# Optimization experiments

Measured on AMD Instinct MI355X. Metric: run time of the kernel, lower is better.

## Reference

```python
import jax, jax.numpy as jnp
import numpy as np

N_USERS = 4096
N_ITEMS = 4096
D = 64  # embedding_dim / out_features
N = N_USERS + N_ITEMS
ALPHA = 0.2  # LeakyReLU slope
NEG_INF = jnp.float32(-9e15)


def setup_inputs() -> dict:
    key = jax.random.key(0)
    ks = jax.random.split(key, 11)
    s = 0.05  # xavier-ish scale
    rn = lambda k, shape: jax.random.normal(k, shape, jnp.float32) * s
    adj = jax.random.randint(ks[0], (N, N), 0, 2, jnp.int32)
    return {
        "adj": adj,
        "user_emb": rn(ks[1], (N_USERS, D)),
        "item_emb": rn(ks[2], (N_ITEMS, D)),
        "W0_w": rn(ks[3], (D, D)), "W0_b": rn(ks[4], (D,)), "a0": rn(ks[5], (2 * D, 1)),
        "W1_w": rn(ks[6], (D, D)), "W1_b": rn(ks[7], (D,)), "a1": rn(ks[8], (2 * D, 1)),
        "out_w": rn(ks[9], (D, D)), "out_b": rn(ks[10], (D,)),
    }


def gat_layer(x, adj, W_w, W_b, a):
    # Wh: [N, D]
    Wh = x @ W_w.T + W_b
    # Original materializes [N,N,2D] concat then matmul with a.
    # Algebraically identical: e_ij = leakyrelu(a1 . Wh_i + a2 . Wh_j)
    src = Wh @ a[:D]          # [N, 1] -> row contribution
    dst = (Wh @ a[D:]).T      # [1, N] -> column contribution
    e = jax.nn.leaky_relu(src + dst, ALPHA)        # [N, N]
    e = jnp.where(adj > 0, e, NEG_INF)
    att = jax.nn.softmax(e, axis=1)                # dropout=0.0 (eval)
    return att @ Wh                                 # [N, D]


def reference(adj, user_emb, item_emb, W0_w, W0_b, a0, W1_w, W1_b, a1, out_w, out_b):
    x = jnp.concatenate([user_emb, item_emb], axis=0)  # [N, D]
    x = jax.nn.relu(gat_layer(x, adj, W0_w, W0_b, a0))
    x = jax.nn.relu(gat_layer(x, adj, W1_w, W1_b, a1))
    u, it = x[:N_USERS], x[N_USERS:]
    return (u @ out_w.T + out_b, it @ out_w.T + out_b)
```

## Files before the change

### kernel.cpp

```cpp
#include <hip/hip_runtime.h>


typedef __attribute__((ext_vector_type(8))) __bf16 bf16x8;
typedef __attribute__((ext_vector_type(4))) float  f32x4;

union Frag {
    bf16x8         v;
    unsigned int   w[4];
    unsigned short h[8];
};

__device__ __forceinline__ unsigned short f2bf(float f) {
    unsigned int u = __float_as_uint(f);
    u += 0x7FFFu + ((u >> 16) & 1u);
    return (unsigned short)(u >> 16);
}

__device__ __forceinline__ void prep_tail(
    float (*xs)[65], float (*Wt)[65], float (*sred)[64], float (*dred)[64],
    const float* __restrict__ W, const float* __restrict__ bias,
    const float* __restrict__ avec,
    unsigned short* __restrict__ WhT, float* __restrict__ sraw,
    float* __restrict__ draw, int tid, int r0)
{
    for (int e = tid; e < 4096; e += 256) {
        int o = e >> 6, c = e & 63;
        Wt[c][o] = W[e];
    }
    __syncthreads();

    int r = tid & 63, chunk = tid >> 6, c0 = chunk * 16;
    float acc[16];
#pragma unroll
    for (int o = 0; o < 16; o++) acc[o] = bias[c0 + o];
    for (int c = 0; c < 64; c++) {
        float xv = xs[r][c];
#pragma unroll
        for (int o = 0; o < 16; o++) acc[o] += xv * Wt[c][c0 + o];
    }

    float sp = 0.f, dp = 0.f;
#pragma unroll
    for (int o = 0; o < 16; o++) {
        sp += acc[o] * avec[c0 + o];
        dp += acc[o] * avec[64 + c0 + o];
    }
    sred[chunk][r] = sp;
    dred[chunk][r] = dp;

#pragma unroll
    for (int o = 0; o < 16; o++)
        WhT[(c0 + o) * 8192 + r0 + r] = f2bf(acc[o]);

    __syncthreads();
    if (tid < 64) {
        int g = r0 + tid;
        sraw[g] = sred[0][tid] + sred[1][tid] + sred[2][tid] + sred[3][tid];
        draw[g] = dred[0][tid] + dred[1][tid] + dred[2][tid] + dred[3][tid];
    }
}

__global__ __launch_bounds__(256) void k_prep0(
    const float* __restrict__ ue, const float* __restrict__ ie,
    const float* __restrict__ W, const float* __restrict__ bias,
    const float* __restrict__ avec,
    unsigned short* __restrict__ WhT,
    float* __restrict__ sraw, float* __restrict__ draw)
{
    __shared__ float xs[64][65];
    __shared__ float Wt[64][65];
    __shared__ float sred[4][64];
    __shared__ float dred[4][64];
    int tid = threadIdx.x, r0 = blockIdx.x * 64;

    for (int e = tid; e < 4096; e += 256) {
        int r = e >> 6, c = e & 63;
        int row = r0 + r;
        xs[r][c] = (row < 4096) ? ue[row * 64 + c] : ie[(row - 4096) * 64 + c];
    }
    prep_tail(xs, Wt, sred, dred, W, bias, avec, WhT, sraw, draw, tid, r0);
}

template <int NS>
__global__ __launch_bounds__(256) void k_prep1(
    const float* __restrict__ numP, const float* __restrict__ denP,
    const float* __restrict__ W, const float* __restrict__ bias,
    const float* __restrict__ avec,
    unsigned short* __restrict__ WhT,
    float* __restrict__ sraw, float* __restrict__ draw)
{
    __shared__ float xs[64][65];
    __shared__ float Wt[64][65];
    __shared__ float sred[4][64];
    __shared__ float dred[4][64];
    __shared__ float dtot[64];
    int tid = threadIdx.x, r0 = blockIdx.x * 64;

    if (tid < 64) {
        float s = 0.f;
#pragma unroll
        for (int p = 0; p < NS; p++) s += denP[p * 8192 + r0 + tid];
        dtot[tid] = fmaxf(s, 1e-20f);
    }
    __syncthreads();
    for (int e = tid; e < 4096; e += 256) {
        int r = e >> 6, c = e & 63;
        float s = 0.f;
#pragma unroll
        for (int p = 0; p < NS; p++)
            s += numP[(size_t)p * 524288 + (r0 + r) * 64 + c];
        float v = s / dtot[r];
        xs[r][c] = v > 0.f ? v : 0.f;
    }
    prep_tail(xs, Wt, sred, dred, W, bias, avec, WhT, sraw, draw, tid, r0);
}

template <int RAW, int NSPLIT>
__global__ __launch_bounds__(256, 8) void k_agg(
    const int* __restrict__ adj, unsigned int* __restrict__ adjbits,
    const unsigned short* __restrict__ WhT,
    const float* __restrict__ sraw, const float* __restrict__ draw,
    float* __restrict__ numP, float* __restrict__ denP)
{
    const int KR = 8192 / NSPLIT;
    int tid  = threadIdx.x;
    int wave = tid >> 6, lane = tid & 63;
    int quad = lane >> 4, l16 = lane & 15;
    int rowblk = blockIdx.x, ks = blockIdx.y;
    int row = rowblk * 64 + wave * 16 + l16;
    int k0  = ks * KR;

    float sv = sraw[row];

    f32x4 accs[4];
    f32x4 accd = {0.f, 0.f, 0.f, 0.f};
#pragma unroll
    for (int nt = 0; nt < 4; nt++) accs[nt] = accd;

    Frag ones;
    ones.w[0] = ones.w[1] = ones.w[2] = ones.w[3] = 0x3F803F80u;

    for (int kb = k0; kb < k0 + KR; kb += 32) {
        int kq = kb + quad * 8;

        unsigned int mask8;
        if constexpr (RAW) {
            const int4* ap = reinterpret_cast<const int4*>(adj + (size_t)row * 8192 + kq);
            int4 a0 = ap[0], a1 = ap[1];
            int ai[8] = {a0.x, a0.y, a0.z, a0.w, a1.x, a1.y, a1.z, a1.w};
            mask8 = 0;
#pragma unroll
            for (int j = 0; j < 8; j++)
                if (ai[j] != 0) mask8 |= (1u << j);
            reinterpret_cast<unsigned char*>(adjbits)[(size_t)row * 1024 + (kb >> 3) + quad] =
                (unsigned char)mask8;
        } else {
            unsigned int word = adjbits[row * 256 + (kb >> 5)];
            mask8 = (word >> (quad * 8)) & 0xFFu;
        }

        float4 dd0 = *reinterpret_cast<const float4*>(draw + kq);
        float4 dd1 = *reinterpret_cast<const float4*>(draw + kq + 4);
        float dv[8] = {dd0.x, dd0.y, dd0.z, dd0.w, dd1.x, dd1.y, dd1.z, dd1.w};

        Frag A;
#pragma unroll
        for (int j = 0; j < 8; j++) {
            float t  = sv + dv[j];
            float lr = t > 0.f ? t : 0.2f * t;
            float w  = ((mask8 >> j) & 1u) ? __expf(lr) : 0.f;
            A.h[j] = f2bf(w);
        }

#pragma unroll
        for (int nt = 0; nt < 4; nt++) {
            Frag B;
            B.v = *reinterpret_cast<const bf16x8*>(WhT + (size_t)(nt * 16 + l16) * 8192 + kq);
            accs[nt] = __builtin_amdgcn_mfma_f32_16x16x32_bf16(A.v, B.v, accs[nt], 0, 0, 0);
        }
        accd = __builtin_amdgcn_mfma_f32_16x16x32_bf16(A.v, ones.v, accd, 0, 0, 0);
    }

    int rbase = rowblk * 64 + wave * 16 + quad * 4;
    size_t nb = (size_t)ks * 524288;
#pragma unroll
    for (int rr = 0; rr < 4; rr++) {
        if (l16 == 0) denP[ks * 8192 + rbase + rr] = accd[rr];
#pragma unroll
        for (int nt = 0; nt < 4; nt++)
            numP[nb + (size_t)(rbase + rr) * 64 + nt * 16 + l16] = accs[nt][rr];
    }
}

template <int NS>
__global__ __launch_bounds__(256) void k_out(
    const float* __restrict__ numP, const float* __restrict__ denP,
    const float* __restrict__ W, const float* __restrict__ bias,
    float* __restrict__ out)
{
    __shared__ float xs[64][65];
    __shared__ float Wt[64][65];
    __shared__ float dtot[64];
    int tid = threadIdx.x, r0 = blockIdx.x * 64;

    if (tid < 64) {
        float s = 0.f;
#pragma unroll
        for (int p = 0; p < NS; p++) s += denP[p * 8192 + r0 + tid];
        dtot[tid] = fmaxf(s, 1e-20f);
    }
    __syncthreads();
    for (int e = tid; e < 4096; e += 256) {
        int r = e >> 6, c = e & 63;
        float s = 0.f;
#pragma unroll
        for (int p = 0; p < NS; p++)
            s += numP[(size_t)p * 524288 + (r0 + r) * 64 + c];
        float v = s / dtot[r];
        xs[r][c] = v > 0.f ? v : 0.f;
    }
    for (int e = tid; e < 4096; e += 256) {
        int o = e >> 6, c = e & 63;
        Wt[c][o] = W[e];
    }
    __syncthreads();

    int r = tid & 63, chunk = tid >> 6, c0 = chunk * 16;
    float acc[16];
#pragma unroll
    for (int o = 0; o < 16; o++) acc[o] = bias[c0 + o];
    for (int c = 0; c < 64; c++) {
        float xv = xs[r][c];
#pragma unroll
        for (int o = 0; o < 16; o++) acc[o] += xv * Wt[c][c0 + o];
    }
#pragma unroll
    for (int o = 0; o < 16; o++)
        out[(r0 + r) * 64 + c0 + o] = acc[o];
}

extern "C" void kernel_launch(void* const* d_in, const int* in_sizes, int n_in,
                              void* d_out, int out_size, void* d_ws, size_t ws_size,
                              hipStream_t stream)
{
    const int*   adj = (const int*)d_in[0];
    const float* ue  = (const float*)d_in[1];
    const float* ie  = (const float*)d_in[2];
    const float* W0w = (const float*)d_in[3];
    const float* W0b = (const float*)d_in[4];
    const float* a0  = (const float*)d_in[5];
    const float* W1w = (const float*)d_in[6];
    const float* W1b = (const float*)d_in[7];
    const float* a1  = (const float*)d_in[8];
    const float* Ow  = (const float*)d_in[9];
    const float* Ob  = (const float*)d_in[10];

    constexpr int NS0 = 16, NS1 = 8;

    char* ws = (char*)d_ws;
    size_t off = 0;
    auto alloc = [&](size_t bytes) -> char* {
        char* p = ws + off;
        off += (bytes + 255) & ~(size_t)255;
        return p;
    };
    float*          numP    = (float*)alloc((size_t)NS0 * 524288 * 4);
    float*          denP    = (float*)alloc((size_t)NS0 * 8192 * 4);
    unsigned int*   adjbits = (unsigned int*)alloc(8192 * 1024);
    unsigned short* WhT0    = (unsigned short*)alloc(64 * 8192 * 2);
    unsigned short* WhT1    = (unsigned short*)alloc(64 * 8192 * 2);
    float* sr0 = (float*)alloc(8192 * 4);
    float* dr0 = (float*)alloc(8192 * 4);
    float* sr1 = (float*)alloc(8192 * 4);
    float* dr1 = (float*)alloc(8192 * 4);

    k_prep0<<<128, 256, 0, stream>>>(ue, ie, W0w, W0b, a0, WhT0, sr0, dr0);
    k_agg<1, NS0><<<dim3(128, NS0), 256, 0, stream>>>(adj, adjbits, WhT0,
                                                      sr0, dr0, numP, denP);
    k_prep1<NS0><<<128, 256, 0, stream>>>(numP, denP, W1w, W1b, a1, WhT1, sr1, dr1);
    k_agg<0, NS1><<<dim3(128, NS1), 256, 0, stream>>>((const int*)nullptr, adjbits, WhT1,
                                                      sr1, dr1, numP, denP);
    k_out<NS1><<<128, 256, 0, stream>>>(numP, denP, Ow, Ob, (float*)d_out);
}
```

Baseline: 573.1 us.

## Factor attention exp into per-node terms, stage Wh in LDS with fp16 MFMA

Rewrites the attention weight as max(exp(s_i)exp(d_j), exp(0.2 s_i)exp(0.2 d_j)), precomputed per node in prep, so the inner loop needs only packed fp16 multiplies and a max instead of a per-element exp. The aggregation kernel now packs the adjacency mask with wave ballots into shared memory, double-buffers Wh tiles in LDS, and uses fp16 MFMA instead of bf16. Layer 0 now uses 8 K-splits instead of 16, and partial outputs are written in a block-contiguous layout through an LDS transpose. The risk is fp16 overflow or underflow of the exponent products when scores are large, and reduced parallelism in layer 0.

```diff
diff --git a/kernel.cpp b/kernel.cpp
--- a/kernel.cpp
+++ b/kernel.cpp
@@ -1,27 +1,28 @@
 #include <hip/hip_runtime.h>
 
 
-typedef __attribute__((ext_vector_type(8))) __bf16 bf16x8;
-typedef __attribute__((ext_vector_type(4))) float  f32x4;
-
-union Frag {
-    bf16x8         v;
-    unsigned int   w[4];
-    unsigned short h[8];
+typedef _Float16 f16x8 __attribute__((ext_vector_type(8)));
+typedef _Float16 f16x2 __attribute__((ext_vector_type(2)));
+typedef __attribute__((ext_vector_type(4))) float f32x4;
+
+union Frag16 {
+    f16x8        v;
+    unsigned int u[4];
 };
-
-__device__ __forceinline__ unsigned short f2bf(float f) {
-    unsigned int u = __float_as_uint(f);
-    u += 0x7FFFu + ((u >> 16) & 1u);
-    return (unsigned short)(u >> 16);
-}
+union HV2 {
+    f16x2        v;
+    _Float16     h[2];
+    unsigned int u;
+};
 
 __device__ __forceinline__ void prep_tail(
     float (*xs)[65], float (*Wt)[65], float (*sred)[64], float (*dred)[64],
     const float* __restrict__ W, const float* __restrict__ bias,
     const float* __restrict__ avec,
-    unsigned short* __restrict__ WhT, float* __restrict__ sraw,
-    float* __restrict__ draw, int tid, int r0)
+    _Float16* __restrict__ WhT,
+    unsigned int* __restrict__ E12,
+    _Float16* __restrict__ F1h, _Float16* __restrict__ F2h,
+    int tid, int r0)
 {
     for (int e = tid; e < 4096; e += 256) {
         int o = e >> 6, c = e & 63;
@@ -50,13 +51,19 @@
 
 #pragma unroll
     for (int o = 0; o < 16; o++)
-        WhT[(c0 + o) * 8192 + r0 + r] = f2bf(acc[o]);
+        WhT[(size_t)(c0 + o) * 8192 + r0 + r] = (_Float16)acc[o];
 
     __syncthreads();
     if (tid < 64) {
         int g = r0 + tid;
-        sraw[g] = sred[0][tid] + sred[1][tid] + sred[2][tid] + sred[3][tid];
-        draw[g] = dred[0][tid] + dred[1][tid] + dred[2][tid] + dred[3][tid];
+        float s = sred[0][tid] + sred[1][tid] + sred[2][tid] + sred[3][tid];
+        float d = dred[0][tid] + dred[1][tid] + dred[2][tid] + dred[3][tid];
+        HV2 e;
+        e.h[0] = (_Float16)__expf(s);
+        e.h[1] = (_Float16)__expf(0.2f * s);
+        E12[g] = e.u;
+        F1h[g] = (_Float16)__expf(d);
+        F2h[g] = (_Float16)__expf(0.2f * d);
     }
 }
 
@@ -64,8 +71,8 @@
     const float* __restrict__ ue, const float* __restrict__ ie,
     const float* __restrict__ W, const float* __restrict__ bias,
     const float* __restrict__ avec,
-    unsigned short* __restrict__ WhT,
-    float* __restrict__ sraw, float* __restrict__ draw)
+    _Float16* __restrict__ WhT, unsigned int* __restrict__ E12,
+    _Float16* __restrict__ F1h, _Float16* __restrict__ F2h)
 {
     __shared__ float xs[64][65];
     __shared__ float Wt[64][65];
@@ -78,7 +85,7 @@
         int row = r0 + r;
         xs[r][c] = (row < 4096) ? ue[row * 64 + c] : ie[(row - 4096) * 64 + c];
     }
-    prep_tail(xs, Wt, sred, dred, W, bias, avec, WhT, sraw, draw, tid, r0);
+    prep_tail(xs, Wt, sred, dred, W, bias, avec, WhT, E12, F1h, F2h, tid, r0);
 }
 
 template <int NS>
@@ -86,8 +93,8 @@
     const float* __restrict__ numP, const float* __restrict__ denP,
     const float* __restrict__ W, const float* __restrict__ bias,
     const float* __restrict__ avec,
-    unsigned short* __restrict__ WhT,
-    float* __restrict__ sraw, float* __restrict__ draw)
+    _Float16* __restrict__ WhT, unsigned int* __restrict__ E12,
+    _Float16* __restrict__ F1h, _Float16* __restrict__ F2h)
 {
     __shared__ float xs[64][65];
     __shared__ float Wt[64][65];
@@ -95,6 +102,7 @@
     __shared__ float dred[4][64];
     __shared__ float dtot[64];
     int tid = threadIdx.x, r0 = blockIdx.x * 64;
+    int rowblk = blockIdx.x;
 
     if (tid < 64) {
         float s = 0.f;
@@ -104,92 +112,194 @@
     }
     __syncthreads();
     for (int e = tid; e < 4096; e += 256) {
-        int r = e >> 6, c = e & 63;
+        int r = e >> 6;
         float s = 0.f;
 #pragma unroll
         for (int p = 0; p < NS; p++)
-            s += numP[(size_t)p * 524288 + (r0 + r) * 64 + c];
+            s += numP[(size_t)(p * 128 + rowblk) * 4096 + e];
         float v = s / dtot[r];
-        xs[r][c] = v > 0.f ? v : 0.f;
-    }
-    prep_tail(xs, Wt, sred, dred, W, bias, avec, WhT, sraw, draw, tid, r0);
-}
-
-template <int RAW, int NSPLIT>
-__global__ __launch_bounds__(256, 8) void k_agg(
-    const int* __restrict__ adj, unsigned int* __restrict__ adjbits,
-    const unsigned short* __restrict__ WhT,
-    const float* __restrict__ sraw, const float* __restrict__ draw,
+        xs[r][e & 63] = v > 0.f ? v : 0.f;
+    }
+    prep_tail(xs, Wt, sred, dred, W, bias, avec, WhT, E12, F1h, F2h, tid, r0);
+}
+
+struct AggSmem {
+    union {
+        _Float16 WhB[64][136];
+        struct {
+            float T[64][68];
+            float denT[64];
+        } ep;
+    } u;
+    unsigned int mkAll[64][36];
+    unsigned int f1All[512];
+    unsigned int f2All[512];
+};
+
+template <int RAW>
+__global__ __launch_bounds__(256) void k_agg(
+    const int* __restrict__ adj, unsigned int* __restrict__ bits,
+    const _Float16* __restrict__ WhT, const unsigned int* __restrict__ E12,
+    const _Float16* __restrict__ F1h, const _Float16* __restrict__ F2h,
     float* __restrict__ numP, float* __restrict__ denP)
 {
-    const int KR = 8192 / NSPLIT;
+    constexpr int CK = 128, NCH = 8;
+    __shared__ AggSmem sm;
+
     int tid  = threadIdx.x;
     int wave = tid >> 6, lane = tid & 63;
     int quad = lane >> 4, l16 = lane & 15;
     int rowblk = blockIdx.x, ks = blockIdx.y;
+    int k0 = ks * (CK * NCH);
+
+    if constexpr (RAW) {
+        for (int r = 0; r < 16; r++) {
+            int row_l = wave * 16 + r;
+            const int* ap = adj + (size_t)(rowblk * 64 + row_l) * 8192 + k0 + lane;
+            int a[16];
+#pragma unroll
+            for (int g = 0; g < 16; g++) a[g] = ap[g * 64];
+            unsigned long long mb[16];
+#pragma unroll
+            for (int g = 0; g < 16; g++) mb[g] = __ballot(a[g] != 0);
+            if (lane == 0) {
+#pragma unroll
+                for (int g = 0; g < 16; g++) {
+                    sm.mkAll[row_l][2 * g]     = (unsigned int)mb[g];
+                    sm.mkAll[row_l][2 * g + 1] = (unsigned int)(mb[g] >> 32);
+                }
+            }
+        }
+        __syncthreads();
+        for (int t = tid; t < 512; t += 256) {
+            int row_l = t >> 3, w4 = (t & 7) * 4;
+            uint4 v = *reinterpret_cast<const uint4*>(&sm.mkAll[row_l][w4]);
+            *reinterpret_cast<uint4*>(
+                bits + (size_t)(rowblk * 64 + row_l) * 256 + ks * 32 + w4) = v;
+        }
+    } else {
+        for (int t = tid; t < 512; t += 256) {
+            int row_l = t >> 3, w4 = (t & 7) * 4;
+            uint4 v = *reinterpret_cast<const uint4*>(
+                bits + (size_t)(rowblk * 64 + row_l) * 256 + ks * 32 + w4);
+            *reinterpret_cast<uint4*>(&sm.mkAll[row_l][w4]) = v;
+        }
+    }
+    if (tid < 128) {
+        uint4 v = *reinterpret_cast<const uint4*>(F1h + k0 + tid * 8);
+        *reinterpret_cast<uint4*>(&sm.f1All[tid * 4]) = v;
+    } else {
+        int t2 = tid - 128;
+        uint4 v = *reinterpret_cast<const uint4*>(F2h + k0 + t2 * 8);
+        *reinterpret_cast<uint4*>(&sm.f2All[t2 * 4]) = v;
+    }
+
+    uint4 P[4];
+#pragma unroll
+    for (int i = 0; i < 4; i++) {
+        int p = tid + 256 * i, f = p >> 4, c8 = (p & 15) * 8;
+        P[i] = *reinterpret_cast<const uint4*>(WhT + (size_t)f * 8192 + k0 + c8);
+    }
+#pragma unroll
+    for (int i = 0; i < 4; i++) {
+        int p = tid + 256 * i, f = p >> 4, c8 = (p & 15) * 8;
+        *reinterpret_cast<uint4*>(&sm.u.WhB[f][c8]) = P[i];
+    }
+    __syncthreads();
+
     int row = rowblk * 64 + wave * 16 + l16;
-    int k0  = ks * KR;
-
-    float sv = sraw[row];
+    int lrow = wave * 16 + l16;
+    unsigned int e12 = E12[row];
+    HV2 e1p, e2p;
+    e1p.u = (e12 & 0xFFFFu);  e1p.u |= e1p.u << 16;
+    e2p.u = (e12 >> 16);      e2p.u |= e2p.u << 16;
 
     f32x4 accs[4];
     f32x4 accd = {0.f, 0.f, 0.f, 0.f};
 #pragma unroll
     for (int nt = 0; nt < 4; nt++) accs[nt] = accd;
 
-    Frag ones;
-    ones.w[0] = ones.w[1] = ones.w[2] = ones.w[3] = 0x3F803F80u;
-
-    for (int kb = k0; kb < k0 + KR; kb += 32) {
-        int kq = kb + quad * 8;
-
-        unsigned int mask8;
-        if constexpr (RAW) {
-            const int4* ap = reinterpret_cast<const int4*>(adj + (size_t)row * 8192 + kq);
-            int4 a0 = ap[0], a1 = ap[1];
-            int ai[8] = {a0.x, a0.y, a0.z, a0.w, a1.x, a1.y, a1.z, a1.w};
-            mask8 = 0;
-#pragma unroll
-            for (int j = 0; j < 8; j++)
-                if (ai[j] != 0) mask8 |= (1u << j);
-            reinterpret_cast<unsigned char*>(adjbits)[(size_t)row * 1024 + (kb >> 3) + quad] =
-                (unsigned char)mask8;
-        } else {
-            unsigned int word = adjbits[row * 256 + (kb >> 5)];
-            mask8 = (word >> (quad * 8)) & 0xFFu;
-        }
-
-        float4 dd0 = *reinterpret_cast<const float4*>(draw + kq);
-        float4 dd1 = *reinterpret_cast<const float4*>(draw + kq + 4);
-        float dv[8] = {dd0.x, dd0.y, dd0.z, dd0.w, dd1.x, dd1.y, dd1.z, dd1.w};
-
-        Frag A;
-#pragma unroll
-        for (int j = 0; j < 8; j++) {
-            float t  = sv + dv[j];
-            float lr = t > 0.f ? t : 0.2f * t;
-            float w  = ((mask8 >> j) & 1u) ? __expf(lr) : 0.f;
-            A.h[j] = f2bf(w);
-        }
-
-#pragma unroll
-        for (int nt = 0; nt < 4; nt++) {
-            Frag B;
-            B.v = *reinterpret_cast<const bf16x8*>(WhT + (size_t)(nt * 16 + l16) * 8192 + kq);
-            accs[nt] = __builtin_amdgcn_mfma_f32_16x16x32_bf16(A.v, B.v, accs[nt], 0, 0, 0);
-        }
-        accd = __builtin_amdgcn_mfma_f32_16x16x32_bf16(A.v, ones.v, accd, 0, 0, 0);
-    }
-
-    int rbase = rowblk * 64 + wave * 16 + quad * 4;
-    size_t nb = (size_t)ks * 524288;
+    Frag16 ones;
+    ones.u[0] = ones.u[1] = ones.u[2] = ones.u[3] = 0x3C003C00u;
+
+    for (int c = 0; c < NCH; c++) {
+        if (c + 1 < NCH) {
+            int kc = k0 + (c + 1) * CK;
+#pragma unroll
+            for (int i = 0; i < 4; i++) {
+                int p = tid + 256 * i, f = p >> 4, c8 = (p & 15) * 8;
+                P[i] = *reinterpret_cast<const uint4*>(
+                    WhT + (size_t)f * 8192 + kc + c8);
+            }
+        }
+
+#pragma unroll
+        for (int kb = 0; kb < CK; kb += 32) {
+            int kq = kb + quad * 8;
+            unsigned int word = sm.mkAll[lrow][c * 4 + (kb >> 5)];
+            unsigned int w8 = word >> (quad * 8);
+
+            int fidx = (c * CK + kq) >> 1;
+            uint4 f1v = *reinterpret_cast<const uint4*>(&sm.f1All[fidx]);
+            uint4 f2v = *reinterpret_cast<const uint4*>(&sm.f2All[fidx]);
+            unsigned int f1a[4] = {f1v.x, f1v.y, f1v.z, f1v.w};
+            unsigned int f2a[4] = {f2v.x, f2v.y, f2v.z, f2v.w};
+
+            Frag16 A;
+#pragma unroll
+            for (int p = 0; p < 4; p++) {
+                HV2 fa, fb, wa;
+                fa.u = f1a[p];
+                fb.u = f2a[p];
+                wa.v = __builtin_elementwise_max(e1p.v * fa.v, e2p.v * fb.v);
+                int s0 = ((int)(w8 << (31 - 2 * p))) >> 31;
+                int s1 = ((int)(w8 << (30 - 2 * p))) >> 31;
+                unsigned int pm = ((unsigned)s0 & 0xFFFFu) | ((unsigned)s1 << 16);
+                A.u[p] = wa.u & pm;
+            }
+
+#pragma unroll
+            for (int nt = 0; nt < 4; nt++) {
+                Frag16 B;
+                B.v = *reinterpret_cast<const f16x8*>(&sm.u.WhB[nt * 16 + l16][kq]);
+                accs[nt] = __builtin_amdgcn_mfma_f32_16x16x32_f16(A.v, B.v,
+                                                                  accs[nt], 0, 0, 0);
+            }
+            accd = __builtin_amdgcn_mfma_f32_16x16x32_f16(A.v, ones.v, accd, 0, 0, 0);
+        }
+
+        if (c + 1 < NCH) {
+            __syncthreads();
+#pragma unroll
+            for (int i = 0; i < 4; i++) {
+                int p = tid + 256 * i, f = p >> 4, c8 = (p & 15) * 8;
+                *reinterpret_cast<uint4*>(&sm.u.WhB[f][c8]) = P[i];
+            }
+            __syncthreads();
+        }
+    }
+
+    __syncthreads();
 #pragma unroll
     for (int rr = 0; rr < 4; rr++) {
-        if (l16 == 0) denP[ks * 8192 + rbase + rr] = accd[rr];
+        int r = wave * 16 + quad * 4 + rr;
 #pragma unroll
         for (int nt = 0; nt < 4; nt++)
-            numP[nb + (size_t)(rbase + rr) * 64 + nt * 16 + l16] = accs[nt][rr];
-    }
+            sm.u.ep.T[r][nt * 16 + l16] = accs[nt][rr];
+        if (l16 == 0) sm.u.ep.denT[r] = accd[rr];
+    }
+    __syncthreads();
+
+    float* dst = numP + (size_t)(ks * 128 + rowblk) * 4096;
+#pragma unroll
+    for (int i = 0; i < 4; i++) {
+        int idx = i * 1024 + tid * 4;
+        int r = idx >> 6, c2 = idx & 63;
+        float4 v = *reinterpret_cast<const float4*>(&sm.u.ep.T[r][c2]);
+        *reinterpret_cast<float4*>(dst + idx) = v;
+    }
+    if (tid < 64)
+        denP[ks * 8192 + rowblk * 64 + tid] = sm.u.ep.denT[tid];
 }
 
 template <int NS>
@@ -202,6 +312,7 @@
     __shared__ float Wt[64][65];
     __shared__ float dtot[64];
     int tid = threadIdx.x, r0 = blockIdx.x * 64;
+    int rowblk = blockIdx.x;
 
     if (tid < 64) {
         float s = 0.f;
@@ -211,13 +322,13 @@
     }
     __syncthreads();
     for (int e = tid; e < 4096; e += 256) {
-        int r = e >> 6, c = e & 63;
+        int r = e >> 6;
         float s = 0.f;
 #pragma unroll
         for (int p = 0; p < NS; p++)
-            s += numP[(size_t)p * 524288 + (r0 + r) * 64 + c];
+            s += numP[(size_t)(p * 128 + rowblk) * 4096 + e];
         float v = s / dtot[r];
-        xs[r][c] = v > 0.f ? v : 0.f;
+        xs[r][e & 63] = v > 0.f ? v : 0.f;
     }
     for (int e = tid; e < 4096; e += 256) {
         int o = e >> 6, c = e & 63;
@@ -255,7 +366,7 @@
     const float* Ow  = (const float*)d_in[9];
     const float* Ob  = (const float*)d_in[10];
 
-    constexpr int NS0 = 16, NS1 = 8;
+    constexpr int NS = 8;
 
     char* ws = (char*)d_ws;
     size_t off = 0;
@@ -264,21 +375,25 @@
         off += (bytes + 255) & ~(size_t)255;
         return p;
     };
-    float*          numP    = (float*)alloc((size_t)NS0 * 524288 * 4);
-    float*          denP    = (float*)alloc((size_t)NS0 * 8192 * 4);
-    unsigned int*   adjbits = (unsigned int*)alloc(8192 * 1024);
-    unsigned short* WhT0    = (unsigned short*)alloc(64 * 8192 * 2);
-    unsigned short* WhT1    = (unsigned short*)alloc(64 * 8192 * 2);
-    float* sr0 = (float*)alloc(8192 * 4);
-    float* dr0 = (float*)alloc(8192 * 4);
-    float* sr1 = (float*)alloc(8192 * 4);
-    float* dr1 = (float*)alloc(8192 * 4);
-
-    k_prep0<<<128, 256, 0, stream>>>(ue, ie, W0w, W0b, a0, WhT0, sr0, dr0);
-    k_agg<1, NS0><<<dim3(128, NS0), 256, 0, stream>>>(adj, adjbits, WhT0,
-                                                      sr0, dr0, numP, denP);
-    k_prep1<NS0><<<128, 256, 0, stream>>>(numP, denP, W1w, W1b, a1, WhT1, sr1, dr1);
-    k_agg<0, NS1><<<dim3(128, NS1), 256, 0, stream>>>((const int*)nullptr, adjbits, WhT1,
-                                                      sr1, dr1, numP, denP);
-    k_out<NS1><<<128, 256, 0, stream>>>(numP, denP, Ow, Ob, (float*)d_out);
-}
+    float*        numP    = (float*)alloc((size_t)NS * 524288 * 4);
+    float*        denP    = (float*)alloc((size_t)NS * 8192 * 4);
+    unsigned int* adjbits = (unsigned int*)alloc(8192 * 1024);
+    _Float16*     WhT0    = (_Float16*)alloc(64 * 8192 * 2);
+    _Float16*     WhT1    = (_Float16*)alloc(64 * 8192 * 2);
+    unsigned int* E12_0   = (unsigned int*)alloc(8192 * 4);
+    unsigned int* E12_1   = (unsigned int*)alloc(8192 * 4);
+    _Float16* F1h0 = (_Float16*)alloc(8192 * 2);
+    _Float16* F2h0 = (_Float16*)alloc(8192 * 2);
+    _Float16* F1h1 = (_Float16*)alloc(8192 * 2);
+    _Float16* F2h1 = (_Float16*)alloc(8192 * 2);
+
+    k_prep0<<<128, 256, 0, stream>>>(ue, ie, W0w, W0b, a0,
+                                     WhT0, E12_0, F1h0, F2h0);
+    k_agg<1><<<dim3(128, NS), 256, 0, stream>>>(adj, adjbits, WhT0, E12_0,
+                                                F1h0, F2h0, numP, denP);
+    k_prep1<NS><<<128, 256, 0, stream>>>(numP, denP, W1w, W1b, a1,
+                                         WhT1, E12_1, F1h1, F2h1);
+    k_agg<0><<<dim3(128, NS), 256, 0, stream>>>(adj, adjbits, WhT1, E12_1,
+                                                F1h1, F2h1, numP, denP);
+    k_out<NS><<<128, 256, 0, stream>>>(numP, denP, Ow, Ob, (float*)d_out);
+}
```

Result: faster. 514.4 us (-10.2%).
